# Kernel optimization log

Hardware: AMD Instinct MI355X
Metric: run time of the kernel (lower is better)

Reference implementation:

```python
import jax, jax.numpy as jnp
import numpy as np

B, HQ, S, D = 2, 16, 2048, 64   # batch, query heads, seq len, head dim
DV = 2 * D                      # value head dim (differential attention)
LAMBDA_INIT = 0.8
EPS = 1e-5
NEG = -1.0e9


def setup_inputs() -> dict:
    key = jax.random.key(0)
    ks = jax.random.split(key, 8)
    return {
        "q": jax.random.normal(ks[0], (B, HQ, S, D), dtype=jnp.float32),
        "k": jax.random.normal(ks[1], (B, HQ, S, D), dtype=jnp.float32),
        "v": jax.random.normal(ks[2], (B, HQ // 2, S, DV), dtype=jnp.float32),
        "lambda_q1": jax.random.normal(ks[3], (D,), dtype=jnp.float32) * 0.1,
        "lambda_k1": jax.random.normal(ks[4], (D,), dtype=jnp.float32) * 0.1,
        "lambda_q2": jax.random.normal(ks[5], (D,), dtype=jnp.float32) * 0.1,
        "lambda_k2": jax.random.normal(ks[6], (D,), dtype=jnp.float32) * 0.1,
        "gn_weight": jnp.ones((HQ * D,), dtype=jnp.float32),
        "gn_bias": jnp.zeros((HQ * D,), dtype=jnp.float32),
    }


def ghostmax(scores):
    # softmax with an implicit extra zero logit per row
    m = jnp.maximum(jnp.max(scores, axis=-1, keepdims=True), 0.0)
    e = jnp.exp(scores - m)
    return e / (jnp.sum(e, axis=-1, keepdims=True) + jnp.exp(-m))


def group_norm(x, weight, bias, num_groups, eps):
    # x: [B, C, S]; normalize each group over (C/G, S) like nn.GroupNorm
    b, c, s = x.shape
    xg = x.reshape(b, num_groups, (c // num_groups) * s)
    mean = jnp.mean(xg, axis=-1, keepdims=True)
    var = jnp.var(xg, axis=-1, keepdims=True)
    xn = ((xg - mean) * jax.lax.rsqrt(var + eps)).reshape(b, c, s)
    return xn * weight[None, :, None] + bias[None, :, None]


def reference(q, k, v, lambda_q1, lambda_k1, lambda_q2, lambda_k2, gn_weight, gn_bias):
    scale = 1.0 / np.sqrt(D).astype(np.float32)
    scores = jnp.einsum("bhqd,bhkd->bhqk", q, k) * scale
    causal = jnp.triu(jnp.full((S, S), NEG, dtype=scores.dtype), k=1)
    scores = scores + causal[None, None]
    w = ghostmax(scores)                                   # [B, HQ, S, S]
    w = w.reshape(B, HQ // 2, 2, S, S)
    lam1 = jnp.exp(jnp.sum(lambda_q1 * lambda_k1))
    lam2 = jnp.exp(jnp.sum(lambda_q2 * lambda_k2))
    lam = lam1 - lam2 + LAMBDA_INIT
    w = w[:, :, 0] - lam * w[:, :, 1]                      # [B, HQ/2, S, S]
    out = jnp.einsum("bhqk,bhkd->bhqd", w, v)              # [B, HQ/2, S, DV]
    out = out.reshape(B, HQ * D, S)                        # faithful to torch reshape
    out = group_norm(out, gn_weight, gn_bias, num_groups=HQ, eps=EPS)
    return out * (1.0 - LAMBDA_INIT)
```

## Files before the change

kernel.cpp:

```cpp
#include <hip/hip_runtime.h>
#include <hip/hip_bf16.h>

constexpr int B_ = 2, HQ_ = 16, HP_ = 8, S_ = 2048, D_ = 64, DV_ = 128;
constexpr float LAMB0 = 0.8f;
constexpr float EPSV = 1e-5f;

constexpr int TQ = 64, TK = 32;
constexpr int KSTR = 72;
constexpr int VSTR = 40;

typedef __attribute__((ext_vector_type(8))) short bf16x8;
typedef __attribute__((ext_vector_type(4))) float f32x4;
typedef __attribute__((ext_vector_type(4))) short short4v;

__device__ __forceinline__ unsigned short f2bf(float x) {
  unsigned u = __float_as_uint(x);
  u += 0x7FFFu + ((u >> 16) & 1u);
  return (unsigned short)(u >> 16);
}
__device__ __forceinline__ float bf2f(unsigned short h) {
  return __uint_as_float((unsigned)h << 16);
}
__device__ __forceinline__ unsigned pack2(unsigned short a, unsigned short b) {
  return (unsigned)a | ((unsigned)b << 16);
}

__launch_bounds__(256, 2)
__global__ void diffattn_fwd(const float* __restrict__ qg, const float* __restrict__ kg,
                             const float* __restrict__ vg,
                             const float* __restrict__ lq1, const float* __restrict__ lk1,
                             const float* __restrict__ lq2, const float* __restrict__ lk2,
                             float* __restrict__ Obuf) {
  __shared__ short Kl[2][2][TK][KSTR];
  __shared__ short Vt[2][DV_][VSTR];

  const int tid = threadIdx.x;
  const int w = tid >> 6;
  const int l = tid & 63;
  const int g = l >> 4;
  const int li = l & 15;

  const int t = blockIdx.x;
  const int bh = t & 15;
  const int b = bh >> 3;
  const int hp = bh & 7;
  const int u = t >> 4;
  const int qt = (u & 1) ? (31 - (u >> 1)) : (u >> 1);
  const int q0 = qt * TQ;
  const int qw = q0 + w * 16;

  float d1 = 0.f, d2 = 0.f;
  for (int i = 0; i < D_; ++i) { d1 += lq1[i] * lk1[i]; d2 += lq2[i] * lk2[i]; }
  const float lam = __expf(d1) - __expf(d2) + LAMB0;

  bf16x8 qhi[2][2], qlo[2][2];
#pragma unroll
  for (int h = 0; h < 2; ++h)
#pragma unroll
    for (int c = 0; c < 2; ++c) {
      const float* p = qg + (((size_t)b * HQ_ + 2 * hp + h) * S_ + qw + li) * D_ + c * 32 + g * 8;
      float4 a = *reinterpret_cast<const float4*>(p);
      float4 bq = *reinterpret_cast<const float4*>(p + 4);
      float xs[8] = {a.x, a.y, a.z, a.w, bq.x, bq.y, bq.z, bq.w};
      union { bf16x8 v; unsigned us[4]; } H, L;
#pragma unroll
      for (int j = 0; j < 4; ++j) {
        unsigned short h0 = f2bf(xs[2 * j]), h1 = f2bf(xs[2 * j + 1]);
        H.us[j] = pack2(h0, h1);
        L.us[j] = pack2(f2bf(xs[2 * j] - bf2f(h0)), f2bf(xs[2 * j + 1] - bf2f(h1)));
      }
      qhi[h][c] = H.v;
      qlo[h][c] = L.v;
    }

  float mreg[2] = {0.f, 0.f};
  float lreg[2] = {1.f, 1.f};
  const f32x4 zero4 = {0.f, 0.f, 0.f, 0.f};
  f32x4 Oacc[2][8];
#pragma unroll
  for (int h = 0; h < 2; ++h)
#pragma unroll
    for (int d = 0; d < 8; ++d) Oacc[h][d] = zero4;

  const int khs = tid >> 7;
  const int ktf = tid & 127;
  const float* kb0 = kg + ((size_t)b * HQ_ + 2 * hp + khs) * S_ * D_;
  const int vdv = tid & 127;
  const int vkq0 = tid >> 7;
  const float* vb0 = vg + ((size_t)b * HP_ + hp) * S_ * DV_ + vdv;

  const int nkt = (q0 + TQ) / TK;
  for (int kt = 0; kt < nkt; ++kt) {
    const int k0 = kt * TK;
    __syncthreads();

    {
      const float* kb = kb0 + (size_t)k0 * D_;
#pragma unroll
      for (int it = 0; it < 4; ++it) {
        int f = ktf + 128 * it;
        int row = f >> 4, c4 = (f & 15) * 4;
        float4 x = *reinterpret_cast<const float4*>(kb + row * D_ + c4);
        unsigned short h0 = f2bf(x.x), h1 = f2bf(x.y), h2 = f2bf(x.z), h3 = f2bf(x.w);
        short4v hi = {(short)h0, (short)h1, (short)h2, (short)h3};
        short4v lo = {(short)f2bf(x.x - bf2f(h0)), (short)f2bf(x.y - bf2f(h1)),
                      (short)f2bf(x.z - bf2f(h2)), (short)f2bf(x.w - bf2f(h3))};
        *reinterpret_cast<short4v*>(&Kl[khs][0][row][c4]) = hi;
        *reinterpret_cast<short4v*>(&Kl[khs][1][row][c4]) = lo;
      }
    }
    {
      const float* vb = vb0 + (size_t)k0 * DV_;
#pragma unroll
      for (int it = 0; it < 4; ++it) {
        int kq = vkq0 + 2 * it;
        float x0 = vb[(size_t)(kq * 4 + 0) * DV_];
        float x1 = vb[(size_t)(kq * 4 + 1) * DV_];
        float x2 = vb[(size_t)(kq * 4 + 2) * DV_];
        float x3 = vb[(size_t)(kq * 4 + 3) * DV_];
        unsigned short h0 = f2bf(x0), h1 = f2bf(x1), h2 = f2bf(x2), h3 = f2bf(x3);
        short4v hi = {(short)h0, (short)h1, (short)h2, (short)h3};
        short4v lo = {(short)f2bf(x0 - bf2f(h0)), (short)f2bf(x1 - bf2f(h1)),
                      (short)f2bf(x2 - bf2f(h2)), (short)f2bf(x3 - bf2f(h3))};
        *reinterpret_cast<short4v*>(&Vt[0][vdv][kq * 4]) = hi;
        *reinterpret_cast<short4v*>(&Vt[1][vdv][kq * 4]) = lo;
      }
    }
    __syncthreads();

    if (k0 > qw + 15) continue;
    const bool needmask = (k0 + TK - 1 > qw);

    bf16x8 Ahi[2], Alo[2];

#pragma unroll
    for (int h = 0; h < 2; ++h) {
      bf16x8 kf[2][2][2];
#pragma unroll
      for (int hl = 0; hl < 2; ++hl)
#pragma unroll
        for (int ms = 0; ms < 2; ++ms)
#pragma unroll
          for (int c = 0; c < 2; ++c)
            kf[hl][ms][c] =
                *reinterpret_cast<const bf16x8*>(&Kl[h][hl][ms * 16 + li][c * 32 + g * 8]);

      f32x4 sT[2] = {zero4, zero4};
      __builtin_amdgcn_s_setprio(1);
#pragma unroll
      for (int ms = 0; ms < 2; ++ms)
#pragma unroll
        for (int c = 0; c < 2; ++c) {
          sT[ms] = __builtin_amdgcn_mfma_f32_16x16x32_bf16(kf[0][ms][c], qhi[h][c], sT[ms], 0, 0, 0);
          sT[ms] = __builtin_amdgcn_mfma_f32_16x16x32_bf16(kf[0][ms][c], qlo[h][c], sT[ms], 0, 0, 0);
          sT[ms] = __builtin_amdgcn_mfma_f32_16x16x32_bf16(kf[1][ms][c], qhi[h][c], sT[ms], 0, 0, 0);
        }
      __builtin_amdgcn_s_setprio(0);

      const int qglob = qw + li;
      float sv[2][4];
#pragma unroll
      for (int ms = 0; ms < 2; ++ms)
#pragma unroll
        for (int r = 0; r < 4; ++r) {
          float v = sT[ms][r] * 0.125f;
          if (needmask && (k0 + ms * 16 + g * 4 + r > qglob)) v = -1e30f;
          sv[ms][r] = v;
        }
      float tmax = fmaxf(fmaxf(fmaxf(sv[0][0], sv[0][1]), fmaxf(sv[0][2], sv[0][3])),
                         fmaxf(fmaxf(sv[1][0], sv[1][1]), fmaxf(sv[1][2], sv[1][3])));
      tmax = fmaxf(tmax, __shfl_xor(tmax, 16));
      tmax = fmaxf(tmax, __shfl_xor(tmax, 32));
      const float mnew = fmaxf(mreg[h], tmax);
      const float fh = __expf(mreg[h] - mnew);
      float p[2][4];
      float psum = 0.f;
#pragma unroll
      for (int ms = 0; ms < 2; ++ms)
#pragma unroll
        for (int r = 0; r < 4; ++r) {
          p[ms][r] = __expf(sv[ms][r] - mnew);
          psum += p[ms][r];
        }
      psum += __shfl_xor(psum, 16);
      psum += __shfl_xor(psum, 32);
      lreg[h] = lreg[h] * fh + psum;
      mreg[h] = mnew;
      if (!__all(fh == 1.0f)) {
        float fr[4];
#pragma unroll
        for (int r = 0; r < 4; ++r) fr[r] = __shfl(fh, 20 * g + r);
#pragma unroll
        for (int d = 0; d < 8; ++d) {
          f32x4 o = Oacc[h][d];
          o[0] *= fr[0]; o[1] *= fr[1]; o[2] *= fr[2]; o[3] *= fr[3];
          Oacc[h][d] = o;
        }
      }

      unsigned ph0a = pack2(f2bf(p[0][0]), f2bf(p[0][1]));
      unsigned ph0b = pack2(f2bf(p[0][2]), f2bf(p[0][3]));
      unsigned ph1a = pack2(f2bf(p[1][0]), f2bf(p[1][1]));
      unsigned ph1b = pack2(f2bf(p[1][2]), f2bf(p[1][3]));
      float pl[2][4];
#pragma unroll
      for (int ms = 0; ms < 2; ++ms)
#pragma unroll
        for (int r = 0; r < 4; ++r) pl[ms][r] = p[ms][r] - bf2f(f2bf(p[ms][r]));
      unsigned pl0a = pack2(f2bf(pl[0][0]), f2bf(pl[0][1]));
      unsigned pl0b = pack2(f2bf(pl[0][2]), f2bf(pl[0][3]));
      unsigned pl1a = pack2(f2bf(pl[1][0]), f2bf(pl[1][1]));
      unsigned pl1b = pack2(f2bf(pl[1][2]), f2bf(pl[1][3]));

      const int srcA = 32 * (g & 1) + li;
      const int srcB = srcA + 16;
      const bool hiMs = (g >> 1) != 0;
      union { bf16x8 v; unsigned us[4]; } AH, AL;
      {
        unsigned a0 = (unsigned)__shfl((int)ph0a, srcA), b0 = (unsigned)__shfl((int)ph1a, srcA);
        unsigned a1 = (unsigned)__shfl((int)ph0b, srcA), b1 = (unsigned)__shfl((int)ph1b, srcA);
        unsigned a2 = (unsigned)__shfl((int)ph0a, srcB), b2 = (unsigned)__shfl((int)ph1a, srcB);
        unsigned a3 = (unsigned)__shfl((int)ph0b, srcB), b3 = (unsigned)__shfl((int)ph1b, srcB);
        AH.us[0] = hiMs ? b0 : a0; AH.us[1] = hiMs ? b1 : a1;
        AH.us[2] = hiMs ? b2 : a2; AH.us[3] = hiMs ? b3 : a3;
      }
      {
        unsigned a0 = (unsigned)__shfl((int)pl0a, srcA), b0 = (unsigned)__shfl((int)pl1a, srcA);
        unsigned a1 = (unsigned)__shfl((int)pl0b, srcA), b1 = (unsigned)__shfl((int)pl1b, srcA);
        unsigned a2 = (unsigned)__shfl((int)pl0a, srcB), b2 = (unsigned)__shfl((int)pl1a, srcB);
        unsigned a3 = (unsigned)__shfl((int)pl0b, srcB), b3 = (unsigned)__shfl((int)pl1b, srcB);
        AL.us[0] = hiMs ? b0 : a0; AL.us[1] = hiMs ? b1 : a1;
        AL.us[2] = hiMs ? b2 : a2; AL.us[3] = hiMs ? b3 : a3;
      }
      Ahi[h] = AH.v;
      Alo[h] = AL.v;
    }

    __builtin_amdgcn_s_setprio(1);
#pragma unroll
    for (int dvt = 0; dvt < 8; ++dvt) {
      bf16x8 vh = *reinterpret_cast<const bf16x8*>(&Vt[0][dvt * 16 + li][g * 8]);
      bf16x8 vl = *reinterpret_cast<const bf16x8*>(&Vt[1][dvt * 16 + li][g * 8]);
#pragma unroll
      for (int h = 0; h < 2; ++h) {
        f32x4 acc = Oacc[h][dvt];
        acc = __builtin_amdgcn_mfma_f32_16x16x32_bf16(Ahi[h], vh, acc, 0, 0, 0);
        acc = __builtin_amdgcn_mfma_f32_16x16x32_bf16(Alo[h], vh, acc, 0, 0, 0);
        acc = __builtin_amdgcn_mfma_f32_16x16x32_bf16(Ahi[h], vl, acc, 0, 0, 0);
        Oacc[h][dvt] = acc;
      }
    }
    __builtin_amdgcn_s_setprio(0);
  }

  float rl0[4], rl1[4];
#pragma unroll
  for (int r = 0; r < 4; ++r) {
    rl0[r] = 1.f / __shfl(lreg[0], 20 * g + r);
    rl1[r] = lam / __shfl(lreg[1], 20 * g + r);
  }
  float* ob = Obuf + ((size_t)(b * HP_ + hp)) * S_ * DV_;
#pragma unroll
  for (int dvt = 0; dvt < 8; ++dvt)
#pragma unroll
    for (int r = 0; r < 4; ++r) {
      float vres = Oacc[0][dvt][r] * rl0[r] - Oacc[1][dvt][r] * rl1[r];
      ob[(size_t)(qw + g * 4 + r) * DV_ + dvt * 16 + li] = vres;
    }
}

__global__ void gn_stats(const float* __restrict__ O, float* __restrict__ stats) {
  const int g = blockIdx.x >> 3;
  const int slice = blockIdx.x & 7;
  const size_t base = (size_t)g * 131072 + (size_t)slice * 16384;
  const int tid = threadIdx.x;
  float sum = 0.f, ss = 0.f;
#pragma unroll 4
  for (int it = 0; it < 16; ++it) {
    int idx = it * 256 + tid;
    float4 x = *reinterpret_cast<const float4*>(O + base + (size_t)idx * 4);
    sum += x.x + x.y + x.z + x.w;
    ss += x.x * x.x + x.y * x.y + x.z * x.z + x.w * x.w;
  }
#pragma unroll
  for (int o = 1; o < 64; o <<= 1) {
    sum += __shfl_xor(sum, o);
    ss += __shfl_xor(ss, o);
  }
  __shared__ float red[8];
  if ((tid & 63) == 0) {
    red[(tid >> 6) * 2] = sum;
    red[(tid >> 6) * 2 + 1] = ss;
  }
  __syncthreads();
  if (tid == 0) {
    atomicAdd(&stats[2 * g + 0], red[0] + red[2] + red[4] + red[6]);
    atomicAdd(&stats[2 * g + 1], red[1] + red[3] + red[5] + red[7]);
  }
}

__global__ void gn_apply(const float* __restrict__ O, const float* __restrict__ stats,
                         const float* __restrict__ gw, const float* __restrict__ gb,
                         float* __restrict__ out) {
  const size_t f = ((size_t)blockIdx.x * 256 + threadIdx.x) * 4;
  const int g = (int)(f >> 17);
  const int sidx = (int)((f >> 7) & 2047);
  const int hp = (int)((f >> 18) & 7);
  const int c = hp * 128 + (sidx >> 4);
  const float mean = stats[2 * g + 0] * (1.f / 131072.f);
  const float var = stats[2 * g + 1] * (1.f / 131072.f) - mean * mean;
  const float sc = rsqrtf(var + EPSV) * gw[c] * 0.2f;
  const float bi = gb[c] * 0.2f;
  float4 x = *reinterpret_cast<const float4*>(O + f);
  float4 y;
  y.x = (x.x - mean) * sc + bi;
  y.y = (x.y - mean) * sc + bi;
  y.z = (x.z - mean) * sc + bi;
  y.w = (x.w - mean) * sc + bi;
  *reinterpret_cast<float4*>(out + f) = y;
}

extern "C" void kernel_launch(void* const* d_in, const int* in_sizes, int n_in,
                              void* d_out, int out_size, void* d_ws, size_t ws_size,
                              hipStream_t stream) {
  const float* q = (const float*)d_in[0];
  const float* k = (const float*)d_in[1];
  const float* v = (const float*)d_in[2];
  const float* lq1 = (const float*)d_in[3];
  const float* lk1 = (const float*)d_in[4];
  const float* lq2 = (const float*)d_in[5];
  const float* lk2 = (const float*)d_in[6];
  const float* gw = (const float*)d_in[7];
  const float* gb = (const float*)d_in[8];
  float* out = (float*)d_out;

  float* Obuf = (float*)d_ws;
  float* stats = (float*)((char*)d_ws + (size_t)B_ * HP_ * S_ * DV_ * sizeof(float));

  hipMemsetAsync(stats, 0, 32 * 2 * sizeof(float), stream);
  diffattn_fwd<<<dim3(512), dim3(256), 0, stream>>>(q, k, v, lq1, lk1, lq2, lk2, Obuf);
  gn_stats<<<dim3(256), dim3(256), 0, stream>>>(Obuf, stats);
  gn_apply<<<dim3(4096), dim3(256), 0, stream>>>(Obuf, stats, gw, gb, out);
}
```

Measured before the change: 321.0 us.

## Stream K from global, double-buffer V, exchange P via LDS, fuse group-norm stats

Each wave now reads K fragments directly from global memory and splits them to bf16 hi/lo in registers, so the shared K tile is gone. V is prefetched into registers and written to a double-buffered LDS tile, which removes one barrier per iteration. P is reshuffled into MFMA operand layout through a small LDS buffer instead of many cross-lane shuffles. The online-softmax max is only raised when it grows by more than 8 (lazy rescale), occupancy is raised to 3 blocks per CU, and group-norm statistics are reduced in the epilogue so the separate stats kernel is dropped. In exchange, K global loads are repeated by every wave, and the lazy max lets exponentials grow up to about e^8.

After: 546.4 us. 70.2% more time.

```diff
diff --git a/kernel.cpp b/kernel.cpp
--- a/kernel.cpp
+++ b/kernel.cpp
@@ -6,7 +6,6 @@
 constexpr float EPSV = 1e-5f;
 
 constexpr int TQ = 64, TK = 32;
-constexpr int KSTR = 72;
 constexpr int VSTR = 40;
 
 typedef __attribute__((ext_vector_type(8))) short bf16x8;
@@ -25,14 +24,15 @@
   return (unsigned)a | ((unsigned)b << 16);
 }
 
-__launch_bounds__(256, 2)
+__launch_bounds__(256, 3)
 __global__ void diffattn_fwd(const float* __restrict__ qg, const float* __restrict__ kg,
                              const float* __restrict__ vg,
                              const float* __restrict__ lq1, const float* __restrict__ lk1,
                              const float* __restrict__ lq2, const float* __restrict__ lk2,
-                             float* __restrict__ Obuf) {
-  __shared__ short Kl[2][2][TK][KSTR];
-  __shared__ short Vt[2][DV_][VSTR];
+                             float* __restrict__ Obuf, float* __restrict__ stats) {
+  __shared__ short Vt[2][2][DV_][VSTR];
+  __shared__ short Pex[4][32][40];
+  __shared__ float redbuf[8];
 
   const int tid = threadIdx.x;
   const int w = tid >> 6;
@@ -82,175 +82,177 @@
 #pragma unroll
     for (int d = 0; d < 8; ++d) Oacc[h][d] = zero4;
 
-  const int khs = tid >> 7;
-  const int ktf = tid & 127;
-  const float* kb0 = kg + ((size_t)b * HQ_ + 2 * hp + khs) * S_ * D_;
   const int vdv = tid & 127;
   const int vkq0 = tid >> 7;
   const float* vb0 = vg + ((size_t)b * HP_ + hp) * S_ * DV_ + vdv;
+  float vreg[16];
+
+  auto issue_v = [&](int k0) {
+    const float* vb = vb0 + (size_t)k0 * DV_;
+#pragma unroll
+    for (int it = 0; it < 4; ++it) {
+      int kq = vkq0 + 2 * it;
+#pragma unroll
+      for (int c = 0; c < 4; ++c) vreg[it * 4 + c] = vb[(size_t)(kq * 4 + c) * DV_];
+    }
+  };
+  auto write_v = [&](int bufp) {
+#pragma unroll
+    for (int it = 0; it < 4; ++it) {
+      int kq = vkq0 + 2 * it;
+      float x0 = vreg[it * 4 + 0], x1 = vreg[it * 4 + 1];
+      float x2 = vreg[it * 4 + 2], x3 = vreg[it * 4 + 3];
+      unsigned short h0 = f2bf(x0), h1 = f2bf(x1), h2 = f2bf(x2), h3 = f2bf(x3);
+      short4v hi = {(short)h0, (short)h1, (short)h2, (short)h3};
+      short4v lo = {(short)f2bf(x0 - bf2f(h0)), (short)f2bf(x1 - bf2f(h1)),
+                    (short)f2bf(x2 - bf2f(h2)), (short)f2bf(x3 - bf2f(h3))};
+      *reinterpret_cast<short4v*>(&Vt[bufp][0][vdv][kq * 4]) = hi;
+      *reinterpret_cast<short4v*>(&Vt[bufp][1][vdv][kq * 4]) = lo;
+    }
+  };
 
   const int nkt = (q0 + TQ) / TK;
+
+  issue_v(0);
+  write_v(0);
+  __syncthreads();
+
   for (int kt = 0; kt < nkt; ++kt) {
     const int k0 = kt * TK;
-    __syncthreads();
-
-    {
-      const float* kb = kb0 + (size_t)k0 * D_;
-#pragma unroll
-      for (int it = 0; it < 4; ++it) {
-        int f = ktf + 128 * it;
-        int row = f >> 4, c4 = (f & 15) * 4;
-        float4 x = *reinterpret_cast<const float4*>(kb + row * D_ + c4);
-        unsigned short h0 = f2bf(x.x), h1 = f2bf(x.y), h2 = f2bf(x.z), h3 = f2bf(x.w);
-        short4v hi = {(short)h0, (short)h1, (short)h2, (short)h3};
-        short4v lo = {(short)f2bf(x.x - bf2f(h0)), (short)f2bf(x.y - bf2f(h1)),
-                      (short)f2bf(x.z - bf2f(h2)), (short)f2bf(x.w - bf2f(h3))};
-        *reinterpret_cast<short4v*>(&Kl[khs][0][row][c4]) = hi;
-        *reinterpret_cast<short4v*>(&Kl[khs][1][row][c4]) = lo;
+    const int p_ = kt & 1;
+
+    if (kt + 1 < nkt) issue_v((kt + 1) * TK);
+
+    if (k0 <= qw + 15) {
+      const bool needmask = (k0 + TK - 1 > qw);
+      const int qglob = qw + li;
+      bf16x8 AH[2], AL[2];
+
+#pragma unroll
+      for (int h = 0; h < 2; ++h) {
+        const float* kb = kg + (((size_t)b * HQ_ + 2 * hp + h) * S_ + k0 + li) * D_ + g * 8;
+        f32x4 sT[2] = {zero4, zero4};
+#pragma unroll
+        for (int ms = 0; ms < 2; ++ms) {
+          float4 kA[4];
+#pragma unroll
+          for (int cc = 0; cc < 2; ++cc) {
+            const float* p = kb + (size_t)(ms * 16) * D_ + cc * 32;
+            kA[cc * 2 + 0] = *reinterpret_cast<const float4*>(p);
+            kA[cc * 2 + 1] = *reinterpret_cast<const float4*>(p + 4);
+          }
+          bf16x8 khi[2], klo[2];
+#pragma unroll
+          for (int cc = 0; cc < 2; ++cc) {
+            float xs[8] = {kA[cc * 2].x,     kA[cc * 2].y,     kA[cc * 2].z,     kA[cc * 2].w,
+                           kA[cc * 2 + 1].x, kA[cc * 2 + 1].y, kA[cc * 2 + 1].z, kA[cc * 2 + 1].w};
+            union { bf16x8 v; unsigned us[4]; } H, L;
+#pragma unroll
+            for (int j = 0; j < 4; ++j) {
+              unsigned short h0 = f2bf(xs[2 * j]), h1 = f2bf(xs[2 * j + 1]);
+              H.us[j] = pack2(h0, h1);
+              L.us[j] = pack2(f2bf(xs[2 * j] - bf2f(h0)), f2bf(xs[2 * j + 1] - bf2f(h1)));
+            }
+            khi[cc] = H.v;
+            klo[cc] = L.v;
+          }
+          __builtin_amdgcn_s_setprio(1);
+#pragma unroll
+          for (int cc = 0; cc < 2; ++cc) {
+            sT[ms] = __builtin_amdgcn_mfma_f32_16x16x32_bf16(khi[cc], qhi[h][cc], sT[ms], 0, 0, 0);
+            sT[ms] = __builtin_amdgcn_mfma_f32_16x16x32_bf16(khi[cc], qlo[h][cc], sT[ms], 0, 0, 0);
+            sT[ms] = __builtin_amdgcn_mfma_f32_16x16x32_bf16(klo[cc], qhi[h][cc], sT[ms], 0, 0, 0);
+          }
+          __builtin_amdgcn_s_setprio(0);
+        }
+
+        float sv[2][4];
+#pragma unroll
+        for (int ms = 0; ms < 2; ++ms)
+#pragma unroll
+          for (int r = 0; r < 4; ++r) {
+            float v = sT[ms][r] * 0.125f;
+            if (needmask && (k0 + ms * 16 + g * 4 + r > qglob)) v = -1e30f;
+            sv[ms][r] = v;
+          }
+        float tmax = fmaxf(fmaxf(fmaxf(sv[0][0], sv[0][1]), fmaxf(sv[0][2], sv[0][3])),
+                           fmaxf(fmaxf(sv[1][0], sv[1][1]), fmaxf(sv[1][2], sv[1][3])));
+        tmax = fmaxf(tmax, __shfl_xor(tmax, 16));
+        tmax = fmaxf(tmax, __shfl_xor(tmax, 32));
+
+        if (__any(tmax > mreg[h] + 8.f)) {
+          const float mnew = fmaxf(mreg[h], tmax);
+          const float fh = __expf(mreg[h] - mnew);
+          mreg[h] = mnew;
+          lreg[h] *= fh;
+          float fr[4];
+#pragma unroll
+          for (int r = 0; r < 4; ++r) fr[r] = __shfl(fh, 20 * g + r);
+#pragma unroll
+          for (int d = 0; d < 8; ++d) {
+            f32x4 o = Oacc[h][d];
+            o[0] *= fr[0]; o[1] *= fr[1]; o[2] *= fr[2]; o[3] *= fr[3];
+            Oacc[h][d] = o;
+          }
+        }
+
+        float p[2][4], psum = 0.f;
+#pragma unroll
+        for (int ms = 0; ms < 2; ++ms)
+#pragma unroll
+          for (int r = 0; r < 4; ++r) {
+            p[ms][r] = __expf(sv[ms][r] - mreg[h]);
+            psum += p[ms][r];
+          }
+        psum += __shfl_xor(psum, 16);
+        psum += __shfl_xor(psum, 32);
+        lreg[h] += psum;
+
+        {
+          union { unsigned uu[2]; short4v s; } W;
+          W.uu[0] = pack2(f2bf(p[0][0]), f2bf(p[0][1]));
+          W.uu[1] = pack2(f2bf(p[0][2]), f2bf(p[0][3]));
+          *reinterpret_cast<short4v*>(&Pex[w][li][g * 4]) = W.s;
+          W.uu[0] = pack2(f2bf(p[1][0]), f2bf(p[1][1]));
+          W.uu[1] = pack2(f2bf(p[1][2]), f2bf(p[1][3]));
+          *reinterpret_cast<short4v*>(&Pex[w][li][16 + g * 4]) = W.s;
+          float pl[2][4];
+#pragma unroll
+          for (int ms = 0; ms < 2; ++ms)
+#pragma unroll
+            for (int r = 0; r < 4; ++r) pl[ms][r] = p[ms][r] - bf2f(f2bf(p[ms][r]));
+          W.uu[0] = pack2(f2bf(pl[0][0]), f2bf(pl[0][1]));
+          W.uu[1] = pack2(f2bf(pl[0][2]), f2bf(pl[0][3]));
+          *reinterpret_cast<short4v*>(&Pex[w][16 + li][g * 4]) = W.s;
+          W.uu[0] = pack2(f2bf(pl[1][0]), f2bf(pl[1][1]));
+          W.uu[1] = pack2(f2bf(pl[1][2]), f2bf(pl[1][3]));
+          *reinterpret_cast<short4v*>(&Pex[w][16 + li][16 + g * 4]) = W.s;
+        }
+        AH[h] = *reinterpret_cast<const bf16x8*>(&Pex[w][li][g * 8]);
+        AL[h] = *reinterpret_cast<const bf16x8*>(&Pex[w][16 + li][g * 8]);
       }
-    }
-    {
-      const float* vb = vb0 + (size_t)k0 * DV_;
-#pragma unroll
-      for (int it = 0; it < 4; ++it) {
-        int kq = vkq0 + 2 * it;
-        float x0 = vb[(size_t)(kq * 4 + 0) * DV_];
-        float x1 = vb[(size_t)(kq * 4 + 1) * DV_];
-        float x2 = vb[(size_t)(kq * 4 + 2) * DV_];
-        float x3 = vb[(size_t)(kq * 4 + 3) * DV_];
-        unsigned short h0 = f2bf(x0), h1 = f2bf(x1), h2 = f2bf(x2), h3 = f2bf(x3);
-        short4v hi = {(short)h0, (short)h1, (short)h2, (short)h3};
-        short4v lo = {(short)f2bf(x0 - bf2f(h0)), (short)f2bf(x1 - bf2f(h1)),
-                      (short)f2bf(x2 - bf2f(h2)), (short)f2bf(x3 - bf2f(h3))};
-        *reinterpret_cast<short4v*>(&Vt[0][vdv][kq * 4]) = hi;
-        *reinterpret_cast<short4v*>(&Vt[1][vdv][kq * 4]) = lo;
-      }
-    }
-    __syncthreads();
-
-    if (k0 > qw + 15) continue;
-    const bool needmask = (k0 + TK - 1 > qw);
-
-    bf16x8 Ahi[2], Alo[2];
-
-#pragma unroll
-    for (int h = 0; h < 2; ++h) {
-      bf16x8 kf[2][2][2];
-#pragma unroll
-      for (int hl = 0; hl < 2; ++hl)
-#pragma unroll
-        for (int ms = 0; ms < 2; ++ms)
-#pragma unroll
-          for (int c = 0; c < 2; ++c)
-            kf[hl][ms][c] =
-                *reinterpret_cast<const bf16x8*>(&Kl[h][hl][ms * 16 + li][c * 32 + g * 8]);
-
-      f32x4 sT[2] = {zero4, zero4};
+
       __builtin_amdgcn_s_setprio(1);
 #pragma unroll
-      for (int ms = 0; ms < 2; ++ms)
-#pragma unroll
-        for (int c = 0; c < 2; ++c) {
-          sT[ms] = __builtin_amdgcn_mfma_f32_16x16x32_bf16(kf[0][ms][c], qhi[h][c], sT[ms], 0, 0, 0);
-          sT[ms] = __builtin_amdgcn_mfma_f32_16x16x32_bf16(kf[0][ms][c], qlo[h][c], sT[ms], 0, 0, 0);
-          sT[ms] = __builtin_amdgcn_mfma_f32_16x16x32_bf16(kf[1][ms][c], qhi[h][c], sT[ms], 0, 0, 0);
-        }
-      __builtin_amdgcn_s_setprio(0);
-
-      const int qglob = qw + li;
-      float sv[2][4];
-#pragma unroll
-      for (int ms = 0; ms < 2; ++ms)
-#pragma unroll
-        for (int r = 0; r < 4; ++r) {
-          float v = sT[ms][r] * 0.125f;
-          if (needmask && (k0 + ms * 16 + g * 4 + r > qglob)) v = -1e30f;
-          sv[ms][r] = v;
-        }
-      float tmax = fmaxf(fmaxf(fmaxf(sv[0][0], sv[0][1]), fmaxf(sv[0][2], sv[0][3])),
-                         fmaxf(fmaxf(sv[1][0], sv[1][1]), fmaxf(sv[1][2], sv[1][3])));
-      tmax = fmaxf(tmax, __shfl_xor(tmax, 16));
-      tmax = fmaxf(tmax, __shfl_xor(tmax, 32));
-      const float mnew = fmaxf(mreg[h], tmax);
-      const float fh = __expf(mreg[h] - mnew);
-      float p[2][4];
-      float psum = 0.f;
-#pragma unroll
-      for (int ms = 0; ms < 2; ++ms)
-#pragma unroll
-        for (int r = 0; r < 4; ++r) {
-          p[ms][r] = __expf(sv[ms][r] - mnew);
-          psum += p[ms][r];
-        }
-      psum += __shfl_xor(psum, 16);
-      psum += __shfl_xor(psum, 32);
-      lreg[h] = lreg[h] * fh + psum;
-      mreg[h] = mnew;
-      if (!__all(fh == 1.0f)) {
-        float fr[4];
-#pragma unroll
-        for (int r = 0; r < 4; ++r) fr[r] = __shfl(fh, 20 * g + r);
-#pragma unroll
-        for (int d = 0; d < 8; ++d) {
-          f32x4 o = Oacc[h][d];
-          o[0] *= fr[0]; o[1] *= fr[1]; o[2] *= fr[2]; o[3] *= fr[3];
-          Oacc[h][d] = o;
+      for (int dvt = 0; dvt < 8; ++dvt) {
+        bf16x8 vh = *reinterpret_cast<const bf16x8*>(&Vt[p_][0][dvt * 16 + li][g * 8]);
+        bf16x8 vl = *reinterpret_cast<const bf16x8*>(&Vt[p_][1][dvt * 16 + li][g * 8]);
+#pragma unroll
+        for (int h = 0; h < 2; ++h) {
+          f32x4 acc = Oacc[h][dvt];
+          acc = __builtin_amdgcn_mfma_f32_16x16x32_bf16(AH[h], vh, acc, 0, 0, 0);
+          acc = __builtin_amdgcn_mfma_f32_16x16x32_bf16(AL[h], vh, acc, 0, 0, 0);
+          acc = __builtin_amdgcn_mfma_f32_16x16x32_bf16(AH[h], vl, acc, 0, 0, 0);
+          Oacc[h][dvt] = acc;
         }
       }
-
-      unsigned ph0a = pack2(f2bf(p[0][0]), f2bf(p[0][1]));
-      unsigned ph0b = pack2(f2bf(p[0][2]), f2bf(p[0][3]));
-      unsigned ph1a = pack2(f2bf(p[1][0]), f2bf(p[1][1]));
-      unsigned ph1b = pack2(f2bf(p[1][2]), f2bf(p[1][3]));
-      float pl[2][4];
-#pragma unroll
-      for (int ms = 0; ms < 2; ++ms)
-#pragma unroll
-        for (int r = 0; r < 4; ++r) pl[ms][r] = p[ms][r] - bf2f(f2bf(p[ms][r]));
-      unsigned pl0a = pack2(f2bf(pl[0][0]), f2bf(pl[0][1]));
-      unsigned pl0b = pack2(f2bf(pl[0][2]), f2bf(pl[0][3]));
-      unsigned pl1a = pack2(f2bf(pl[1][0]), f2bf(pl[1][1]));
-      unsigned pl1b = pack2(f2bf(pl[1][2]), f2bf(pl[1][3]));
-
-      const int srcA = 32 * (g & 1) + li;
-      const int srcB = srcA + 16;
-      const bool hiMs = (g >> 1) != 0;
-      union { bf16x8 v; unsigned us[4]; } AH, AL;
-      {
-        unsigned a0 = (unsigned)__shfl((int)ph0a, srcA), b0 = (unsigned)__shfl((int)ph1a, srcA);
-        unsigned a1 = (unsigned)__shfl((int)ph0b, srcA), b1 = (unsigned)__shfl((int)ph1b, srcA);
-        unsigned a2 = (unsigned)__shfl((int)ph0a, srcB), b2 = (unsigned)__shfl((int)ph1a, srcB);
-        unsigned a3 = (unsigned)__shfl((int)ph0b, srcB), b3 = (unsigned)__shfl((int)ph1b, srcB);
-        AH.us[0] = hiMs ? b0 : a0; AH.us[1] = hiMs ? b1 : a1;
-        AH.us[2] = hiMs ? b2 : a2; AH.us[3] = hiMs ? b3 : a3;
-      }
-      {
-        unsigned a0 = (unsigned)__shfl((int)pl0a, srcA), b0 = (unsigned)__shfl((int)pl1a, srcA);
-        unsigned a1 = (unsigned)__shfl((int)pl0b, srcA), b1 = (unsigned)__shfl((int)pl1b, srcA);
-        unsigned a2 = (unsigned)__shfl((int)pl0a, srcB), b2 = (unsigned)__shfl((int)pl1a, srcB);
-        unsigned a3 = (unsigned)__shfl((int)pl0b, srcB), b3 = (unsigned)__shfl((int)pl1b, srcB);
-        AL.us[0] = hiMs ? b0 : a0; AL.us[1] = hiMs ? b1 : a1;
-        AL.us[2] = hiMs ? b2 : a2; AL.us[3] = hiMs ? b3 : a3;
-      }
-      Ahi[h] = AH.v;
-      Alo[h] = AL.v;
-    }
-
-    __builtin_amdgcn_s_setprio(1);
-#pragma unroll
-    for (int dvt = 0; dvt < 8; ++dvt) {
-      bf16x8 vh = *reinterpret_cast<const bf16x8*>(&Vt[0][dvt * 16 + li][g * 8]);
-      bf16x8 vl = *reinterpret_cast<const bf16x8*>(&Vt[1][dvt * 16 + li][g * 8]);
-#pragma unroll
-      for (int h = 0; h < 2; ++h) {
-        f32x4 acc = Oacc[h][dvt];
-        acc = __builtin_amdgcn_mfma_f32_16x16x32_bf16(Ahi[h], vh, acc, 0, 0, 0);
-        acc = __builtin_amdgcn_mfma_f32_16x16x32_bf16(Alo[h], vh, acc, 0, 0, 0);
-        acc = __builtin_amdgcn_mfma_f32_16x16x32_bf16(Ahi[h], vl, acc, 0, 0, 0);
-        Oacc[h][dvt] = acc;
-      }
-    }
-    __builtin_amdgcn_s_setprio(0);
+      __builtin_amdgcn_s_setprio(0);
+    }
+
+    if (kt + 1 < nkt) {
+      write_v((kt + 1) & 1);
+      __syncthreads();
+    }
   }
 
   float rl0[4], rl1[4];
@@ -260,42 +262,30 @@
     rl1[r] = lam / __shfl(lreg[1], 20 * g + r);
   }
   float* ob = Obuf + ((size_t)(b * HP_ + hp)) * S_ * DV_;
+  float lsum = 0.f, lss = 0.f;
 #pragma unroll
   for (int dvt = 0; dvt < 8; ++dvt)
 #pragma unroll
     for (int r = 0; r < 4; ++r) {
       float vres = Oacc[0][dvt][r] * rl0[r] - Oacc[1][dvt][r] * rl1[r];
       ob[(size_t)(qw + g * 4 + r) * DV_ + dvt * 16 + li] = vres;
-    }
-}
-
-__global__ void gn_stats(const float* __restrict__ O, float* __restrict__ stats) {
-  const int g = blockIdx.x >> 3;
-  const int slice = blockIdx.x & 7;
-  const size_t base = (size_t)g * 131072 + (size_t)slice * 16384;
-  const int tid = threadIdx.x;
-  float sum = 0.f, ss = 0.f;
-#pragma unroll 4
-  for (int it = 0; it < 16; ++it) {
-    int idx = it * 256 + tid;
-    float4 x = *reinterpret_cast<const float4*>(O + base + (size_t)idx * 4);
-    sum += x.x + x.y + x.z + x.w;
-    ss += x.x * x.x + x.y * x.y + x.z * x.z + x.w * x.w;
-  }
+      lsum += vres;
+      lss += vres * vres;
+    }
 #pragma unroll
   for (int o = 1; o < 64; o <<= 1) {
-    sum += __shfl_xor(sum, o);
-    ss += __shfl_xor(ss, o);
-  }
-  __shared__ float red[8];
-  if ((tid & 63) == 0) {
-    red[(tid >> 6) * 2] = sum;
-    red[(tid >> 6) * 2 + 1] = ss;
+    lsum += __shfl_xor(lsum, o);
+    lss += __shfl_xor(lss, o);
+  }
+  if (l == 0) {
+    redbuf[w * 2] = lsum;
+    redbuf[w * 2 + 1] = lss;
   }
   __syncthreads();
   if (tid == 0) {
-    atomicAdd(&stats[2 * g + 0], red[0] + red[2] + red[4] + red[6]);
-    atomicAdd(&stats[2 * g + 1], red[1] + red[3] + red[5] + red[7]);
+    const int region = ((b * HP_ + hp) << 1) | (q0 >= 1024 ? 1 : 0);
+    atomicAdd(&stats[2 * region + 0], redbuf[0] + redbuf[2] + redbuf[4] + redbuf[6]);
+    atomicAdd(&stats[2 * region + 1], redbuf[1] + redbuf[3] + redbuf[5] + redbuf[7]);
   }
 }
 
@@ -337,8 +327,7 @@
   float* Obuf = (float*)d_ws;
   float* stats = (float*)((char*)d_ws + (size_t)B_ * HP_ * S_ * DV_ * sizeof(float));
 
-  hipMemsetAsync(stats, 0, 32 * 2 * sizeof(float), stream);
-  diffattn_fwd<<<dim3(512), dim3(256), 0, stream>>>(q, k, v, lq1, lk1, lq2, lk2, Obuf);
-  gn_stats<<<dim3(256), dim3(256), 0, stream>>>(Obuf, stats);
+  hipMemsetAsync(stats, 0, 64 * sizeof(float), stream);
+  diffattn_fwd<<<dim3(512), dim3(256), 0, stream>>>(q, k, v, lq1, lk1, lq2, lk2, Obuf, stats);
   gn_apply<<<dim3(4096), dim3(256), 0, stream>>>(Obuf, stats, gw, gb, out);
 }
```
